# Kernel optimization log

Measured on AMD Instinct MI355X. Metric: run time of the kernel, lower is better.

Reference implementation:

```python
import jax, jax.numpy as jnp
import numpy as np

N, E, T, Q, G = 50000, 800000, 1000000, 1000000, 4096
L, H, D, HID, ED = 3, 8, 16, 128, 16
EPS = 1e-8


def setup_inputs() -> dict:
    key = jax.random.key(0)
    ks = jax.random.split(key, 20)
    inp = {
        "x": jax.random.normal(ks[0], (N, HID), jnp.float32),
        "pos": jax.random.normal(ks[1], (N, 3), jnp.float32),
        "edge_attr": jax.random.normal(ks[2], (E, ED), jnp.float32),
        "temps": jax.random.uniform(ks[3], (G, 1), jnp.float32),
        "edge_index": jax.random.randint(ks[4], (2, E), 0, N, jnp.int32),
        "triple_index": jax.random.randint(ks[5], (3, T), 0, N, jnp.int32),
        "quadra_index": jax.random.randint(ks[6], (4, Q), 0, N, jnp.int32),
        "batch": jnp.sort(jax.random.randint(ks[7], (N,), 0, G, jnp.int32)),
        "W": jax.random.normal(ks[8], (L, HID, HID), jnp.float32) * 0.08,
        "a_e": jax.random.normal(ks[9], (L, H, 2 * D + 1), jnp.float32) * 0.1,
        "a_t": jax.random.normal(ks[10], (L, H, 2 * D + 1), jnp.float32) * 0.1,
        "a_q": jax.random.normal(ks[11], (L, H, 2 * D + 1), jnp.float32) * 0.1,
        "We": jax.random.normal(ks[12], (L, ED, H), jnp.float32) * 0.1,
        "W1": jax.random.normal(ks[13], (2 * HID + 1, 256), jnp.float32) * 0.06,
        "b1": jnp.zeros((256,), jnp.float32),
        "W2": jax.random.normal(ks[14], (256, 256), jnp.float32) * 0.06,
        "b2": jnp.zeros((256,), jnp.float32),
        "W3": jax.random.normal(ks[15], (256, 1), jnp.float32) * 0.06,
        "b3": jnp.zeros((1,), jnp.float32),
    }
    return inp


def _seg_softmax(logits, seg, n):
    # numerically stable segment softmax over destination nodes
    m = jax.ops.segment_max(logits, seg, num_segments=n)
    m = jnp.where(jnp.isfinite(m), m, 0.0)
    e = jnp.exp(logits - m[seg])
    s = jax.ops.segment_sum(e, seg, num_segments=n)
    return e / (s[seg] + 1e-16)


def _hop(hh, src, dst, geom, a, bias=None):
    # hh: [N,H,D]; gather-attend-scatter for one interaction order
    q, k = hh[dst], hh[src]                      # [M,H,D]
    logits = jnp.einsum('mhd,hd->mh', q, a[:, :D]) \
           + jnp.einsum('mhd,hd->mh', k, a[:, D:2 * D]) \
           + geom[:, None] * a[:, 2 * D]
    if bias is not None:
        logits = logits + bias
    logits = jax.nn.leaky_relu(logits, 0.2)
    alpha = _seg_softmax(logits, dst, hh.shape[0])  # [M,H]
    return jax.ops.segment_sum(k * alpha[..., None], dst, num_segments=hh.shape[0])


def _geom_features(pos, edge_index, triple_index, quadra_index):
    # edge distance
    d = jnp.linalg.norm(pos[edge_index[0]] - pos[edge_index[1]] + EPS, axis=-1)
    # triple angle cos at center node j of (i,j,k)
    i, j, k = triple_index
    u, v = pos[i] - pos[j], pos[k] - pos[j]
    cos_a = (u * v).sum(-1) / (jnp.linalg.norm(u, axis=-1) * jnp.linalg.norm(v, axis=-1) + EPS)
    # quadra dihedral cos of (p0,p1,p2,p3)
    p0, p1, p2, p3 = pos[quadra_index[0]], pos[quadra_index[1]], pos[quadra_index[2]], pos[quadra_index[3]]
    b1, b2, b3 = p1 - p0, p2 - p1, p3 - p2
    n1, n2 = jnp.cross(b1, b2), jnp.cross(b2, b3)
    cos_d = (n1 * n2).sum(-1) / (jnp.linalg.norm(n1, axis=-1) * jnp.linalg.norm(n2, axis=-1) + EPS)
    return d, cos_a, cos_d


def reference(x, pos, edge_attr, temps, edge_index, triple_index, quadra_index, batch,
              W, a_e, a_t, a_q, We, W1, b1, W2, b2, W3, b3):
    d, cos_a, cos_d = _geom_features(pos, edge_index, triple_index, quadra_index)
    e_src, e_dst = edge_index[1], edge_index[0]
    t_src, t_dst = triple_index[2], triple_index[0]
    q_src, q_dst = quadra_index[3], quadra_index[0]
    h = x
    for l in range(L):
        hl = h @ W[l]                              # [N,HID]
        hh = hl.reshape(N, H, D)
        bias_e = edge_attr @ We[l]                 # [E,H]
        agg = _hop(hh, e_src, e_dst, d, a_e[l], bias_e) \
            + _hop(hh, t_src, t_dst, cos_a, a_t[l]) \
            + _hop(hh, q_src, q_dst, cos_d, a_q[l])
        h = jax.nn.elu(hl + agg.reshape(N, HID))
    # readout: sum + max pooling per graph, concat temperature scalar
    s = jax.ops.segment_sum(h, batch, num_segments=G)
    mx = jax.ops.segment_max(h, batch, num_segments=G)
    mx = jnp.where(jnp.isfinite(mx), mx, 0.0)
    mol = jnp.concatenate([s, mx, temps], axis=-1)  # [G, 2*HID+1]
    hdn = jax.nn.elu(mol @ W1 + b1)
    hdn = jax.nn.elu(hdn @ W2 + b2)
    return hdn @ W3 + b3
```

## Files before the change

### kernel.cpp

```cpp
#include <hip/hip_runtime.h>
#include <hip/hip_fp16.h>

#define NN 50000
#define EE 800000
#define TT 1000000
#define QQ 1000000
#define GG 4096
#define HID 128
#define NH 8
#define DH 16
#define CAPC 96

#define TILE 2048
#define KPT 8
#define NB 196
#define NBG 392

typedef unsigned int u32;
typedef unsigned int u32x4 __attribute__((ext_vector_type(4)));

__device__ __forceinline__ float eluf(float x){ return x > 0.f ? x : expm1f(x); }

__device__ __forceinline__ u32 pack_sg(int src, float g){
  return ((u32)src << 16) | (u32)__half_as_ushort(__float2half(g));
}

__global__ void k_count3(const int* __restrict__ ei, const int* __restrict__ ti, const int* __restrict__ qi,
                         int* __restrict__ cnt){
  int i = blockIdx.x*blockDim.x + threadIdx.x;
  if (i < EE) atomicAdd(&cnt[ei[i]], 1);
  else if (i < EE+TT) atomicAdd(&cnt[NN + ti[i-EE]], 1);
  else if (i < EE+TT+QQ) atomicAdd(&cnt[2*NN + qi[i-EE-TT]], 1);
}

__global__ __launch_bounds__(1024) void k_scan4(const int* __restrict__ cnt,
    int* __restrict__ off_e, int* __restrict__ off_t, int* __restrict__ off_q,
    int* __restrict__ cur_e, int* __restrict__ cur_t, int* __restrict__ cur_q,
    const int* __restrict__ batch, int* __restrict__ goff){
  int b = blockIdx.x, t = threadIdx.x;
  if (b == 3){
    for (int g=t; g<=GG; g+=1024){
      int lo=0, hi=NN;
      while (lo<hi){ int mid=(lo+hi)>>1; if (batch[mid]<g) lo=mid+1; else hi=mid; }
      goff[g]=lo;
    }
    return;
  }
  __shared__ int part[1024];
  const int* c = cnt + b*NN;
  int* off = (b==0)?off_e:(b==1)?off_t:off_q;
  int* cur = (b==0)?cur_e:(b==1)?cur_t:cur_q;
  int chunk = (NN + 1023) >> 10;
  int s0 = t*chunk, s1 = min(NN, s0+chunk);
  int sum = 0;
  for (int i=s0;i<s1;i++) sum += c[i];
  part[t] = sum;
  __syncthreads();
  for (int d=1; d<1024; d<<=1){
    int v = (t>=d) ? part[t-d] : 0;
    __syncthreads();
    part[t] += v;
    __syncthreads();
  }
  int run = (t==0) ? 0 : part[t-1];
  for (int i=s0;i<s1;i++){ off[i]=run; cur[i]=run; run += c[i]; }
  if (t==0) off[NN] = part[1023];
}

__global__ void k_fillE(const float* __restrict__ pos, const float* __restrict__ edge_attr,
    const int* __restrict__ ei, const float* __restrict__ We,
    int* __restrict__ cur_e, u32* __restrict__ eRec){
  int i = blockIdx.x*blockDim.x + threadIdx.x;
  if (i >= EE) return;
  int dn = ei[i], sn = ei[EE+i];
  float dx = pos[dn*3+0]-pos[sn*3+0]+1e-8f;
  float dy = pos[dn*3+1]-pos[sn*3+1]+1e-8f;
  float dz = pos[dn*3+2]-pos[sn*3+2]+1e-8f;
  float d = sqrtf(dx*dx+dy*dy+dz*dz);
  int p = atomicAdd(&cur_e[dn], 1);
  const float4* s = (const float4*)(edge_attr + (size_t)i*16);
  float4 v0=s[0], v1=s[1], v2=s[2], v3=s[3];
  float a[16] = {v0.x,v0.y,v0.z,v0.w, v1.x,v1.y,v1.z,v1.w,
                 v2.x,v2.y,v2.z,v2.w, v3.x,v3.y,v3.z,v3.w};
  u32x4 r[4];
  r[0][0] = pack_sg(sn, d); r[0][1]=0; r[0][2]=0; r[0][3]=0;
  #pragma unroll
  for (int l=0; l<3; l++){
    const float* Wel = We + l*DH*NH;
    #pragma unroll
    for (int hp=0; hp<4; hp++){
      float sa=0.f, sb=0.f;
      #pragma unroll
      for (int c=0;c<16;c++){
        sa = fmaf(a[c], Wel[c*NH + 2*hp],     sa);
        sb = fmaf(a[c], Wel[c*NH + 2*hp + 1], sb);
      }
      __half2 hh = __floats2half2_rn(sa, sb);
      r[1+l][hp] = *(u32*)&hh;
    }
  }
  u32x4* dst4 = (u32x4*)(eRec + (size_t)p*16);
  dst4[0]=r[0]; dst4[1]=r[1]; dst4[2]=r[2]; dst4[3]=r[3];
}

__global__ __launch_bounds__(256) void k_fillTQ_A(const float* __restrict__ pos,
    const int* __restrict__ ti, const int* __restrict__ qi,
    const int* __restrict__ off_t, const int* __restrict__ off_q,
    u32* __restrict__ gcur, uint2* __restrict__ stg){
  __shared__ u32 s_sg[TILE];
  __shared__ u32 s_dw[TILE];
  __shared__ u32 s_cnt[NBG];
  __shared__ u32 s_scan[512];
  __shared__ u32 s_gb[NBG];
  int t = threadIdx.x;
  size_t tile0 = (size_t)blockIdx.x * TILE;
  for (int i=t;i<NBG;i+=256) s_cnt[i]=0;
  __syncthreads();
  u32 my_sg[KPT], my_dw[KPT], my_rank[KPT]; int my_bg[KPT];
  #pragma unroll
  for (int k=0;k<KPT;k++){
    size_t idx = tile0 + (size_t)k*256 + t;
    my_bg[k] = -1;
    if (idx < (size_t)TT+QQ){
      int dst, src; float g;
      int typeq = (idx >= (size_t)TT);
      if (!typeq){
        int m = (int)idx;
        int ia=ti[m], jb=ti[TT+m], kc=ti[2*TT+m];
        float ux=pos[ia*3+0]-pos[jb*3+0], uy=pos[ia*3+1]-pos[jb*3+1], uz=pos[ia*3+2]-pos[jb*3+2];
        float vx=pos[kc*3+0]-pos[jb*3+0], vy=pos[kc*3+1]-pos[jb*3+1], vz=pos[kc*3+2]-pos[jb*3+2];
        float num = ux*vx+uy*vy+uz*vz;
        float den = sqrtf(ux*ux+uy*uy+uz*uz)*sqrtf(vx*vx+vy*vy+vz*vz) + 1e-8f;
        g = num/den; dst = ia; src = kc;
      } else {
        int m = (int)(idx - TT);
        int p0=qi[m], p1=qi[QQ+m], p2=qi[2*QQ+m], p3=qi[3*QQ+m];
        float b1x=pos[p1*3+0]-pos[p0*3+0], b1y=pos[p1*3+1]-pos[p0*3+1], b1z=pos[p1*3+2]-pos[p0*3+2];
        float b2x=pos[p2*3+0]-pos[p1*3+0], b2y=pos[p2*3+1]-pos[p1*3+1], b2z=pos[p2*3+2]-pos[p1*3+2];
        float b3x=pos[p3*3+0]-pos[p2*3+0], b3y=pos[p3*3+1]-pos[p2*3+1], b3z=pos[p3*3+2]-pos[p2*3+2];
        float n1x=b1y*b2z-b1z*b2y, n1y=b1z*b2x-b1x*b2z, n1z=b1x*b2y-b1y*b2x;
        float n2x=b2y*b3z-b2z*b3y, n2y=b2z*b3x-b2x*b3z, n2z=b2x*b3y-b2y*b3x;
        float num = n1x*n2x+n1y*n2y+n1z*n2z;
        float den = sqrtf(n1x*n1x+n1y*n1y+n1z*n1z)*sqrtf(n2x*n2x+n2y*n2y+n2z*n2z) + 1e-8f;
        g = num/den; dst = p0; src = p3;
      }
      int bg = (typeq?NB:0) + (dst>>8);
      my_sg[k] = pack_sg(src, g);
      my_dw[k] = (u32)dst | ((u32)typeq<<20);
      my_bg[k] = bg;
      my_rank[k] = atomicAdd(&s_cnt[bg], 1u);
    }
  }
  __syncthreads();
  int i0=t, i1=t+256;
  s_scan[i0] = (i0<NBG)? s_cnt[i0] : 0u;
  s_scan[i1] = (i1<NBG)? s_cnt[i1] : 0u;
  __syncthreads();
  for (int d=1; d<512; d<<=1){
    u32 a0 = (i0>=d)? s_scan[i0-d] : 0u;
    u32 a1 = (i1>=d)? s_scan[i1-d] : 0u;
    __syncthreads();
    s_scan[i0]+=a0; s_scan[i1]+=a1;
    __syncthreads();
  }
  u32 total = s_scan[NBG-1];
  #pragma unroll
  for (int k=0;k<KPT;k++){
    if (my_bg[k]>=0){
      u32 slot = s_scan[my_bg[k]] - s_cnt[my_bg[k]] + my_rank[k];
      s_sg[slot]=my_sg[k]; s_dw[slot]=my_dw[k];
    }
  }
  for (int i=t;i<NBG;i+=256)
    s_gb[i] = s_cnt[i] ? atomicAdd(&gcur[i], s_cnt[i]) : 0u;
  __syncthreads();
  for (u32 j=t; j<total; j+=256){
    u32 dw = s_dw[j];
    int typeq = (dw>>20)&1;
    int dst = dw & 0xFFFFF;
    int bg = (typeq?NB:0) + (dst>>8);
    u32 rank = j - (s_scan[bg]-s_cnt[bg]);
    int w0 = (typeq? bg-NB : bg)*256;
    size_t sbase = typeq ? (size_t)TT + (size_t)off_q[w0] : (size_t)off_t[w0];
    stg[sbase + s_gb[bg] + rank] = make_uint2(s_sg[j], dw);
  }
}

__global__ __launch_bounds__(256) void k_fillTQ_B(const uint2* __restrict__ stg,
    const int* __restrict__ off_t, const int* __restrict__ off_q,
    u32* __restrict__ csg_t, u32* __restrict__ csg_q){
  __shared__ int curL[256];
  int b = blockIdx.x, t = threadIdx.x;
  int typeq = (b>=NB);
  int bl = typeq? b-NB : b;
  const int* off = typeq? off_q : off_t;
  u32* csg = typeq? csg_q : csg_t;
  int w0 = bl*256, w1 = min(w0+256, NN);
  int s0 = off[w0], s1 = off[w1];
  for (int i=t; i<w1-w0; i+=256) curL[i] = off[w0+i];
  __syncthreads();
  size_t sb = (typeq? (size_t)TT : 0) + (size_t)s0;
  int cnt = s1 - s0;
  for (int i=t; i<cnt; i+=256){
    uint2 r = stg[sb+i];
    int dst = r.y & 0xFFFFF;
    int p = atomicAdd(&curL[dst-w0], 1);
    csg[p] = r.x;
  }
}

#define GR 16
__global__ __launch_bounds__(128) void k_gemm(const float* __restrict__ A, const float* __restrict__ W,
                                              __half* __restrict__ B16){
  int col = threadIdx.x;
  int r0 = blockIdx.x * GR;
  const float* Ab = A + (size_t)r0*HID;
  float acc[GR];
  #pragma unroll
  for (int r=0;r<GR;r++) acc[r]=0.f;
  #pragma unroll 4
  for (int k=0;k<HID;k++){
    float wv = W[k*HID+col];
    #pragma unroll
    for (int r=0;r<GR;r++) acc[r] = fmaf(Ab[r*HID+k], wv, acc[r]);
  }
  #pragma unroll
  for (int r=0;r<GR;r++) B16[(size_t)(r0+r)*HID+col] = __float2half(acc[r]);
}

__global__ void k_proj(const __half* __restrict__ hl16,
    const float* __restrict__ ae, const float* __restrict__ at, const float* __restrict__ aq,
    float* __restrict__ qa_e, float* __restrict__ ka_e,
    float* __restrict__ qa_t, float* __restrict__ ka_t,
    float* __restrict__ qa_q, float* __restrict__ ka_q){
  int i = blockIdx.x*blockDim.x + threadIdx.x;
  if (i >= NN*NH) return;
  int h = i & 7; int n = i >> 3;
  const __half2* v2 = (const __half2*)(hl16 + (size_t)n*HID + h*DH);
  float x[DH];
  #pragma unroll
  for (int d2=0; d2<8; d2++){ float2 f = __half22float2(v2[d2]); x[2*d2]=f.x; x[2*d2+1]=f.y; }
  const float* Ae = ae + h*33; const float* At_ = at + h*33; const float* Aq = aq + h*33;
  float s0=0,s1=0,s2=0,s3=0,s4=0,s5=0;
  #pragma unroll
  for (int d=0; d<DH; d++){
    s0 = fmaf(x[d], Ae[d],      s0);  s1 = fmaf(x[d], Ae[DH+d],  s1);
    s2 = fmaf(x[d], At_[d],     s2);  s3 = fmaf(x[d], At_[DH+d], s3);
    s4 = fmaf(x[d], Aq[d],      s4);  s5 = fmaf(x[d], Aq[DH+d],  s5);
  }
  qa_e[i]=s0; ka_e[i]=s1; qa_t[i]=s2; ka_t[i]=s3; qa_q[i]=s4; ka_q[i]=s5;
}

__device__ __forceinline__ void gather_acc(const __half* __restrict__ hh16,
    const int* __restrict__ srcs, const float* __restrict__ es,
    int cnt, int w, int hg, int l, float& a0, float& a1){
  int m = w;
  for (; m+8 <= cnt; m += 8){
    int s0=srcs[m], s1=srcs[m+2], s2=srcs[m+4], s3=srcs[m+6];
    float e0=es[m*NH+hg], e1=es[(m+2)*NH+hg], e2=es[(m+4)*NH+hg], e3=es[(m+6)*NH+hg];
    float2 f0 = __half22float2(*(const __half2*)&hh16[(size_t)s0*HID + 2*l]);
    float2 f1 = __half22float2(*(const __half2*)&hh16[(size_t)s1*HID + 2*l]);
    float2 f2 = __half22float2(*(const __half2*)&hh16[(size_t)s2*HID + 2*l]);
    float2 f3 = __half22float2(*(const __half2*)&hh16[(size_t)s3*HID + 2*l]);
    a0 = fmaf(f0.x, e0, a0); a1 = fmaf(f0.y, e0, a1);
    a0 = fmaf(f1.x, e1, a0); a1 = fmaf(f1.y, e1, a1);
    a0 = fmaf(f2.x, e2, a0); a1 = fmaf(f2.y, e2, a1);
    a0 = fmaf(f3.x, e3, a0); a1 = fmaf(f3.y, e3, a1);
  }
  for (; m < cnt; m += 2){
    int s0 = srcs[m];
    float e0 = es[m*NH+hg];
    float2 f0 = __half22float2(*(const __half2*)&hh16[(size_t)s0*HID + 2*l]);
    a0 = fmaf(f0.x, e0, a0); a1 = fmaf(f0.y, e0, a1);
  }
}

__global__ __launch_bounds__(128) void k_hop3(
    const int* __restrict__ off_e, const int* __restrict__ off_t, const int* __restrict__ off_q,
    const u32* __restrict__ eRec,
    const u32* __restrict__ csg_t, const u32* __restrict__ csg_q,
    const float* __restrict__ qa_e, const float* __restrict__ ka_e,
    const float* __restrict__ qa_t, const float* __restrict__ ka_t,
    const float* __restrict__ qa_q, const float* __restrict__ ka_q,
    const float* __restrict__ ae, const float* __restrict__ at, const float* __restrict__ aq,
    const __half* __restrict__ hh16, const __half* __restrict__ hlr16, float* __restrict__ hout,
    int L){
  __shared__ float sh_e[3][CAPC*NH];
  __shared__ int   sh_src[3][CAPC];
  __shared__ float sh_geom[3][CAPC];
  __shared__ float sh_s[3*NH];
  __shared__ float sh_qa[3*NH];
  __shared__ float sh_coef[3*NH];
  int n = blockIdx.x, t = threadIdx.x;
  int w = t >> 6, l = t & 63;
  if (t < 24){
    int p = t>>3, h = t&7;
    const float* a  = (p==0)?ae:(p==1)?at:aq;
    const float* qa = (p==0)?qa_e:(p==1)?qa_t:qa_q;
    sh_coef[t] = a[h*33+32];
    sh_qa[t]   = qa[n*NH+h];
    sh_s[t]    = 0.f;
  }
  int st_e = off_e[n], de = off_e[n+1]-st_e;
  int st_t = off_t[n], dt = off_t[n+1]-st_t;
  int st_q = off_q[n], dq = off_q[n+1]-st_q;
  __syncthreads();
  float aE0=0,aE1=0,aT0=0,aT1=0,aQ0=0,aQ1=0;
  int h  = t & 7;
  int hg = l >> 3;
  const __half* eRecH = (const __half*)eRec;
  int maxd = max(de, max(dt, dq));
  for (int base=0; base<maxd; base+=CAPC){
    int ce = min(CAPC, de-base); if (ce<0) ce=0;
    int ct = min(CAPC, dt-base); if (ct<0) ct=0;
    int cq = min(CAPC, dq-base); if (cq<0) cq=0;
    if (t < ce){ u32 v = eRec[(size_t)(st_e+base+t)*16]; sh_src[0][t]=(int)(v>>16); sh_geom[0][t]=__half2float(__ushort_as_half((unsigned short)(v&0xFFFFu))); }
    if (t < ct){ u32 v = csg_t[st_t+base+t]; sh_src[1][t]=(int)(v>>16); sh_geom[1][t]=__half2float(__ushort_as_half((unsigned short)(v&0xFFFFu))); }
    if (t < cq){ u32 v = csg_q[st_q+base+t]; sh_src[2][t]=(int)(v>>16); sh_geom[2][t]=__half2float(__ushort_as_half((unsigned short)(v&0xFFFFu))); }
    __syncthreads();
    float dE=0.f, dT=0.f, dQ=0.f;
    for (int i=t; i<ce*NH; i+=128){
      int m = i>>3;
      float lg = sh_qa[h] + ka_e[sh_src[0][m]*NH+h] + sh_geom[0][m]*sh_coef[h]
               + __half2float(eRecH[(size_t)(st_e+base+m)*32 + 8 + 8*L + h]);
      lg = lg>=0.f ? lg : 0.2f*lg;
      float e = __expf(lg);
      sh_e[0][i] = e; dE += e;
    }
    for (int i=t; i<ct*NH; i+=128){
      int m = i>>3;
      float lg = sh_qa[8+h] + ka_t[sh_src[1][m]*NH+h] + sh_geom[1][m]*sh_coef[8+h];
      lg = lg>=0.f ? lg : 0.2f*lg;
      float e = __expf(lg);
      sh_e[1][i] = e; dT += e;
    }
    for (int i=t; i<cq*NH; i+=128){
      int m = i>>3;
      float lg = sh_qa[16+h] + ka_q[sh_src[2][m]*NH+h] + sh_geom[2][m]*sh_coef[16+h];
      lg = lg>=0.f ? lg : 0.2f*lg;
      float e = __expf(lg);
      sh_e[2][i] = e; dQ += e;
    }
    dE += __shfl_xor(dE, 8); dE += __shfl_xor(dE, 16); dE += __shfl_xor(dE, 32);
    dT += __shfl_xor(dT, 8); dT += __shfl_xor(dT, 16); dT += __shfl_xor(dT, 32);
    dQ += __shfl_xor(dQ, 8); dQ += __shfl_xor(dQ, 16); dQ += __shfl_xor(dQ, 32);
    if (l < 8){
      atomicAdd(&sh_s[l], dE);
      atomicAdd(&sh_s[8+l], dT);
      atomicAdd(&sh_s[16+l], dQ);
    }
    __syncthreads();
    gather_acc(hh16, sh_src[0], sh_e[0], ce, w, hg, l, aE0, aE1);
    gather_acc(hh16, sh_src[1], sh_e[1], ct, w, hg, l, aT0, aT1);
    gather_acc(hh16, sh_src[2], sh_e[2], cq, w, hg, l, aQ0, aQ1);
    __syncthreads();
  }
  float* red = &sh_e[0][0];
  *(float2*)&red[(0*2+w)*128 + 2*l] = make_float2(aE0, aE1);
  *(float2*)&red[(1*2+w)*128 + 2*l] = make_float2(aT0, aT1);
  *(float2*)&red[(2*2+w)*128 + 2*l] = make_float2(aQ0, aQ1);
  __syncthreads();
  int ho = t >> 4;
  float outv = (red[t]       + red[128+t]) / (sh_s[ho]    + 1e-16f)
             + (red[256+t]   + red[384+t]) / (sh_s[8+ho]  + 1e-16f)
             + (red[512+t]   + red[640+t]) / (sh_s[16+ho] + 1e-16f);
  size_t oi = (size_t)n*HID + t;
  hout[oi] = eluf(__half2float(hlr16[oi]) + outv);
}

__global__ __launch_bounds__(128) void k_pool(const float* __restrict__ h, const int* __restrict__ goff,
                                              float* __restrict__ gs, float* __restrict__ gmx){
  int g = blockIdx.x, t = threadIdx.x;
  int s = goff[g], e = goff[g+1];
  float sum = 0.f, mx = -INFINITY;
  for (int n=s; n<e; n++){
    float v = h[(size_t)n*HID+t];
    sum += v; mx = fmaxf(mx, v);
  }
  gs[(size_t)g*HID+t] = sum;
  gmx[(size_t)g*HID+t] = (s < e) ? mx : 0.f;
}

#define GPB 8
#define MSTR 260
__global__ __launch_bounds__(256) void k_mlp(const float* __restrict__ gs, const float* __restrict__ gmx,
    const float* __restrict__ temps,
    const float* __restrict__ W1, const float* __restrict__ b1,
    const float* __restrict__ W2, const float* __restrict__ b2,
    const float* __restrict__ W3, const float* __restrict__ b3,
    float* __restrict__ out){
  __shared__ float mol[GPB][MSTR];
  __shared__ float hd[GPB][MSTR];
  int g0 = blockIdx.x*GPB, t = threadIdx.x;
  for (int i=t; i<GPB*HID; i+=256){
    int g=i>>7, d=i&127;
    mol[g][d]     = gs[(size_t)(g0+g)*HID+d];
    mol[g][128+d] = gmx[(size_t)(g0+g)*HID+d];
  }
  if (t < GPB){ mol[t][256]=temps[g0+t]; mol[t][257]=0.f; mol[t][258]=0.f; mol[t][259]=0.f; }
  __syncthreads();
  float acc[GPB];
  #pragma unroll
  for (int g=0;g<GPB;g++) acc[g]=b1[t];
  for (int k0=0;k0<256;k0+=4){
    float w0=W1[(size_t)(k0+0)*256+t], w1=W1[(size_t)(k0+1)*256+t];
    float w2=W1[(size_t)(k0+2)*256+t], w3=W1[(size_t)(k0+3)*256+t];
    #pragma unroll
    for (int g=0;g<GPB;g++){
      float4 m4 = *(const float4*)&mol[g][k0];
      acc[g] = fmaf(m4.x,w0, fmaf(m4.y,w1, fmaf(m4.z,w2, fmaf(m4.w,w3, acc[g]))));
    }
  }
  { float wl=W1[(size_t)256*256+t];
    #pragma unroll
    for (int g=0;g<GPB;g++) acc[g]=fmaf(mol[g][256],wl,acc[g]); }
  #pragma unroll
  for (int g=0;g<GPB;g++) hd[g][t]=eluf(acc[g]);
  __syncthreads();
  #pragma unroll
  for (int g=0;g<GPB;g++) acc[g]=b2[t];
  for (int k0=0;k0<256;k0+=4){
    float w0=W2[(size_t)(k0+0)*256+t], w1=W2[(size_t)(k0+1)*256+t];
    float w2=W2[(size_t)(k0+2)*256+t], w3=W2[(size_t)(k0+3)*256+t];
    #pragma unroll
    for (int g=0;g<GPB;g++){
      float4 h4 = *(const float4*)&hd[g][k0];
      acc[g] = fmaf(h4.x,w0, fmaf(h4.y,w1, fmaf(h4.z,w2, fmaf(h4.w,w3, acc[g]))));
    }
  }
  float w3v = W3[t];
  #pragma unroll
  for (int g=0;g<GPB;g++) mol[g][t] = eluf(acc[g])*w3v;
  __syncthreads();
  int g = t >> 5, j = t & 31;
  float s = 0.f;
  for (int i=j; i<256; i+=32) s += mol[g][i];
  #pragma unroll
  for (int d=16; d>0; d>>=1) s += __shfl_down(s, d, 32);
  if (j == 0) out[g0+g] = s + b3[0];
}

extern "C" void kernel_launch(void* const* d_in, const int* in_sizes, int n_in,
                              void* d_out, int out_size, void* d_ws, size_t ws_size,
                              hipStream_t stream){
  const float* x         = (const float*)d_in[0];
  const float* pos       = (const float*)d_in[1];
  const float* edge_attr = (const float*)d_in[2];
  const float* temps     = (const float*)d_in[3];
  const int*   ei        = (const int*)d_in[4];
  const int*   ti        = (const int*)d_in[5];
  const int*   qi        = (const int*)d_in[6];
  const int*   batch     = (const int*)d_in[7];
  const float* W         = (const float*)d_in[8];
  const float* a_e       = (const float*)d_in[9];
  const float* a_t       = (const float*)d_in[10];
  const float* a_q       = (const float*)d_in[11];
  const float* We        = (const float*)d_in[12];
  const float* W1        = (const float*)d_in[13];
  const float* b1        = (const float*)d_in[14];
  const float* W2        = (const float*)d_in[15];
  const float* b2        = (const float*)d_in[16];
  const float* W3        = (const float*)d_in[17];
  const float* b3        = (const float*)d_in[18];
  float* out = (float*)d_out;

  char* base = (char*)d_ws; size_t woff = 0;
  auto alloc = [&](size_t bytes)->void*{
    void* p = base + woff;
    woff = (woff + bytes + 255) & ~(size_t)255;
    return p;
  };
  float*  hbuf   = (float*)alloc((size_t)NN*HID*4);
  __half* hl16   = (__half*)alloc((size_t)NN*HID*2);
  float*  qa_e   = (float*)alloc((size_t)NN*NH*4);
  float*  ka_e   = (float*)alloc((size_t)NN*NH*4);
  float*  qa_t   = (float*)alloc((size_t)NN*NH*4);
  float*  ka_t   = (float*)alloc((size_t)NN*NH*4);
  float*  qa_q   = (float*)alloc((size_t)NN*NH*4);
  float*  ka_q   = (float*)alloc((size_t)NN*NH*4);
  u32*    eRec   = (u32*)alloc((size_t)EE*64);
  u32*    csg_t  = (u32*)alloc((size_t)TT*4);
  u32*    csg_q  = (u32*)alloc((size_t)QQ*4);
  uint2*  stg    = (uint2*)alloc((size_t)(TT+QQ)*8);
  float*  gs     = (float*)alloc((size_t)GG*HID*4);
  float*  gmx    = (float*)alloc((size_t)GG*HID*4);
  int*    cnt    = (int*)alloc((size_t)3*NN*4);
  u32*    gcur   = (u32*)alloc((size_t)NBG*4);
  int*    off_e  = (int*)alloc((size_t)(NN+1)*4);
  int*    off_t  = (int*)alloc((size_t)(NN+1)*4);
  int*    off_q  = (int*)alloc((size_t)(NN+1)*4);
  int*    cur_e  = (int*)alloc((size_t)NN*4);
  int*    cur_t  = (int*)alloc((size_t)NN*4);
  int*    cur_q  = (int*)alloc((size_t)NN*4);
  int*    goff   = (int*)alloc((size_t)(GG+1)*4);

  hipMemsetAsync(cnt, 0, (size_t)3*NN*4, stream);
  hipMemsetAsync(gcur, 0, (size_t)NBG*4, stream);
  int tot = EE+TT+QQ;
  k_count3<<<(tot+255)/256,256,0,stream>>>(ei, ti, qi, cnt);
  k_scan4<<<4,1024,0,stream>>>(cnt, off_e, off_t, off_q, cur_e, cur_t, cur_q, batch, goff);
  k_fillE<<<(EE+255)/256,256,0,stream>>>(pos, edge_attr, ei, We, cur_e, eRec);
  k_fillTQ_A<<<(TT+QQ+TILE-1)/TILE,256,0,stream>>>(pos, ti, qi, off_t, off_q, gcur, stg);
  k_fillTQ_B<<<NBG,256,0,stream>>>(stg, off_t, off_q, csg_t, csg_q);

  for (int l=0; l<3; l++){
    const float* hin = (l==0) ? x : hbuf;
    k_gemm<<<NN/GR,128,0,stream>>>(hin, W + (size_t)l*HID*HID, hl16);
    k_proj<<<(NN*NH+255)/256,256,0,stream>>>(hl16, a_e+l*264, a_t+l*264, a_q+l*264,
                                             qa_e, ka_e, qa_t, ka_t, qa_q, ka_q);
    k_hop3<<<NN,128,0,stream>>>(off_e, off_t, off_q, eRec, csg_t, csg_q,
                                qa_e, ka_e, qa_t, ka_t, qa_q, ka_q,
                                a_e+l*264, a_t+l*264, a_q+l*264,
                                hl16, hl16, hbuf, l);
  }

  k_pool<<<GG,128,0,stream>>>(hbuf, goff, gs, gmx);
  k_mlp<<<GG/GPB,256,0,stream>>>(gs, gmx, temps, W1, b1, W2, b2, W3, b3, out);
}
```

Measured before the change: 1.188 ms.

## Process each node with a single wavefront, dropping block-wide syncs in hop kernel

```diff
diff --git a/kernel.cpp b/kernel.cpp
--- a/kernel.cpp
+++ b/kernel.cpp
@@ -9,7 +9,7 @@
 #define HID 128
 #define NH 8
 #define DH 16
-#define CAPC 96
+#define CAP 64
 
 #define TILE 2048
 #define KPT 8
@@ -251,31 +251,68 @@
   qa_e[i]=s0; ka_e[i]=s1; qa_t[i]=s2; ka_t[i]=s3; qa_q[i]=s4; ka_q[i]=s5;
 }
 
-__device__ __forceinline__ void gather_acc(const __half* __restrict__ hh16,
-    const int* __restrict__ srcs, const float* __restrict__ es,
-    int cnt, int w, int hg, int l, float& a0, float& a1){
-  int m = w;
-  for (; m+8 <= cnt; m += 8){
-    int s0=srcs[m], s1=srcs[m+2], s2=srcs[m+4], s3=srcs[m+6];
-    float e0=es[m*NH+hg], e1=es[(m+2)*NH+hg], e2=es[(m+4)*NH+hg], e3=es[(m+6)*NH+hg];
-    float2 f0 = __half22float2(*(const __half2*)&hh16[(size_t)s0*HID + 2*l]);
-    float2 f1 = __half22float2(*(const __half2*)&hh16[(size_t)s1*HID + 2*l]);
-    float2 f2 = __half22float2(*(const __half2*)&hh16[(size_t)s2*HID + 2*l]);
-    float2 f3 = __half22float2(*(const __half2*)&hh16[(size_t)s3*HID + 2*l]);
-    a0 = fmaf(f0.x, e0, a0); a1 = fmaf(f0.y, e0, a1);
-    a0 = fmaf(f1.x, e1, a0); a1 = fmaf(f1.y, e1, a1);
-    a0 = fmaf(f2.x, e2, a0); a1 = fmaf(f2.y, e2, a1);
-    a0 = fmaf(f3.x, e3, a0); a1 = fmaf(f3.y, e3, a1);
-  }
-  for (; m < cnt; m += 2){
-    int s0 = srcs[m];
-    float e0 = es[m*NH+hg];
-    float2 f0 = __half22float2(*(const __half2*)&hh16[(size_t)s0*HID + 2*l]);
-    a0 = fmaf(f0.x, e0, a0); a1 = fmaf(f0.y, e0, a1);
-  }
-}
-
-__global__ __launch_bounds__(128) void k_hop3(
+template<int EB>
+__device__ __forceinline__ void hop_wave(
+    int st, int deg, const u32* __restrict__ csg, const u32* __restrict__ eRec, int L4,
+    const float* __restrict__ ka, const float* __restrict__ qa, const float* __restrict__ acoef,
+    const __half* __restrict__ hh16, float* __restrict__ sa, int n, int l, int hg,
+    float& o0, float& o1){
+  float4 qv0 = *(const float4*)(qa + (size_t)n*8);
+  float4 qv1 = *(const float4*)(qa + (size_t)n*8 + 4);
+  float qa8[8] = {qv0.x,qv0.y,qv0.z,qv0.w,qv1.x,qv1.y,qv1.z,qv1.w};
+  float cf[8];
+  #pragma unroll
+  for (int h=0;h<8;h++) cf[h] = acoef[h*33+32];
+  float acc0=0.f, acc1=0.f, dsum=0.f;
+  for (int base=0; base<deg; base+=CAP){
+    int c = min(CAP, deg-base);
+    u32 sg = 0;
+    if (l < c){
+      size_t idx = (size_t)(st+base+l);
+      float bias8[8] = {0,0,0,0,0,0,0,0};
+      if (EB){
+        sg = eRec[idx*16];
+        u32x4 br = *(const u32x4*)(eRec + idx*16 + 4 + L4);
+        #pragma unroll
+        for (int h=0;h<8;h++){
+          u32 bw = br[h>>1];
+          unsigned short us = (h&1)? (unsigned short)(bw>>16) : (unsigned short)(bw&0xFFFFu);
+          bias8[h] = __half2float(__ushort_as_half(us));
+        }
+      } else {
+        sg = csg[idx];
+      }
+      int src = (int)(sg>>16);
+      float g = __half2float(__ushort_as_half((unsigned short)(sg&0xFFFFu)));
+      float4 k0 = *(const float4*)(ka + (size_t)src*8);
+      float4 k1 = *(const float4*)(ka + (size_t)src*8 + 4);
+      float ka8[8] = {k0.x,k0.y,k0.z,k0.w,k1.x,k1.y,k1.z,k1.w};
+      #pragma unroll
+      for (int h=0;h<8;h++){
+        float lg = qa8[h] + ka8[h] + g*cf[h] + bias8[h];
+        lg = lg>=0.f ? lg : 0.2f*lg;
+        sa[l*9+h] = __expf(lg);
+      }
+    }
+    __builtin_amdgcn_wave_barrier();
+    #pragma unroll 4
+    for (int m=0; m<c; ++m){
+      float am = sa[m*9+hg];
+      u32 sv = __shfl(sg, m);
+      int src = (int)(sv>>16);
+      float2 f = __half22float2(*(const __half2*)&hh16[(size_t)src*HID + 2*l]);
+      dsum += am;
+      acc0 = fmaf(f.x, am, acc0);
+      acc1 = fmaf(f.y, am, acc1);
+    }
+    __builtin_amdgcn_wave_barrier();
+  }
+  float inv = 1.f/(dsum + 1e-16f);
+  o0 = fmaf(acc0, inv, o0);
+  o1 = fmaf(acc1, inv, o1);
+}
+
+__global__ __launch_bounds__(256) void k_hop3(
     const int* __restrict__ off_e, const int* __restrict__ off_t, const int* __restrict__ off_q,
     const u32* __restrict__ eRec,
     const u32* __restrict__ csg_t, const u32* __restrict__ csg_q,
@@ -285,87 +322,23 @@
     const float* __restrict__ ae, const float* __restrict__ at, const float* __restrict__ aq,
     const __half* __restrict__ hh16, const __half* __restrict__ hlr16, float* __restrict__ hout,
     int L){
-  __shared__ float sh_e[3][CAPC*NH];
-  __shared__ int   sh_src[3][CAPC];
-  __shared__ float sh_geom[3][CAPC];
-  __shared__ float sh_s[3*NH];
-  __shared__ float sh_qa[3*NH];
-  __shared__ float sh_coef[3*NH];
-  int n = blockIdx.x, t = threadIdx.x;
-  int w = t >> 6, l = t & 63;
-  if (t < 24){
-    int p = t>>3, h = t&7;
-    const float* a  = (p==0)?ae:(p==1)?at:aq;
-    const float* qa = (p==0)?qa_e:(p==1)?qa_t:qa_q;
-    sh_coef[t] = a[h*33+32];
-    sh_qa[t]   = qa[n*NH+h];
-    sh_s[t]    = 0.f;
-  }
-  int st_e = off_e[n], de = off_e[n+1]-st_e;
-  int st_t = off_t[n], dt = off_t[n+1]-st_t;
-  int st_q = off_q[n], dq = off_q[n+1]-st_q;
-  __syncthreads();
-  float aE0=0,aE1=0,aT0=0,aT1=0,aQ0=0,aQ1=0;
-  int h  = t & 7;
-  int hg = l >> 3;
-  const __half* eRecH = (const __half*)eRec;
-  int maxd = max(de, max(dt, dq));
-  for (int base=0; base<maxd; base+=CAPC){
-    int ce = min(CAPC, de-base); if (ce<0) ce=0;
-    int ct = min(CAPC, dt-base); if (ct<0) ct=0;
-    int cq = min(CAPC, dq-base); if (cq<0) cq=0;
-    if (t < ce){ u32 v = eRec[(size_t)(st_e+base+t)*16]; sh_src[0][t]=(int)(v>>16); sh_geom[0][t]=__half2float(__ushort_as_half((unsigned short)(v&0xFFFFu))); }
-    if (t < ct){ u32 v = csg_t[st_t+base+t]; sh_src[1][t]=(int)(v>>16); sh_geom[1][t]=__half2float(__ushort_as_half((unsigned short)(v&0xFFFFu))); }
-    if (t < cq){ u32 v = csg_q[st_q+base+t]; sh_src[2][t]=(int)(v>>16); sh_geom[2][t]=__half2float(__ushort_as_half((unsigned short)(v&0xFFFFu))); }
-    __syncthreads();
-    float dE=0.f, dT=0.f, dQ=0.f;
-    for (int i=t; i<ce*NH; i+=128){
-      int m = i>>3;
-      float lg = sh_qa[h] + ka_e[sh_src[0][m]*NH+h] + sh_geom[0][m]*sh_coef[h]
-               + __half2float(eRecH[(size_t)(st_e+base+m)*32 + 8 + 8*L + h]);
-      lg = lg>=0.f ? lg : 0.2f*lg;
-      float e = __expf(lg);
-      sh_e[0][i] = e; dE += e;
-    }
-    for (int i=t; i<ct*NH; i+=128){
-      int m = i>>3;
-      float lg = sh_qa[8+h] + ka_t[sh_src[1][m]*NH+h] + sh_geom[1][m]*sh_coef[8+h];
-      lg = lg>=0.f ? lg : 0.2f*lg;
-      float e = __expf(lg);
-      sh_e[1][i] = e; dT += e;
-    }
-    for (int i=t; i<cq*NH; i+=128){
-      int m = i>>3;
-      float lg = sh_qa[16+h] + ka_q[sh_src[2][m]*NH+h] + sh_geom[2][m]*sh_coef[16+h];
-      lg = lg>=0.f ? lg : 0.2f*lg;
-      float e = __expf(lg);
-      sh_e[2][i] = e; dQ += e;
-    }
-    dE += __shfl_xor(dE, 8); dE += __shfl_xor(dE, 16); dE += __shfl_xor(dE, 32);
-    dT += __shfl_xor(dT, 8); dT += __shfl_xor(dT, 16); dT += __shfl_xor(dT, 32);
-    dQ += __shfl_xor(dQ, 8); dQ += __shfl_xor(dQ, 16); dQ += __shfl_xor(dQ, 32);
-    if (l < 8){
-      atomicAdd(&sh_s[l], dE);
-      atomicAdd(&sh_s[8+l], dT);
-      atomicAdd(&sh_s[16+l], dQ);
-    }
-    __syncthreads();
-    gather_acc(hh16, sh_src[0], sh_e[0], ce, w, hg, l, aE0, aE1);
-    gather_acc(hh16, sh_src[1], sh_e[1], ct, w, hg, l, aT0, aT1);
-    gather_acc(hh16, sh_src[2], sh_e[2], cq, w, hg, l, aQ0, aQ1);
-    __syncthreads();
-  }
-  float* red = &sh_e[0][0];
-  *(float2*)&red[(0*2+w)*128 + 2*l] = make_float2(aE0, aE1);
-  *(float2*)&red[(1*2+w)*128 + 2*l] = make_float2(aT0, aT1);
-  *(float2*)&red[(2*2+w)*128 + 2*l] = make_float2(aQ0, aQ1);
-  __syncthreads();
-  int ho = t >> 4;
-  float outv = (red[t]       + red[128+t]) / (sh_s[ho]    + 1e-16f)
-             + (red[256+t]   + red[384+t]) / (sh_s[8+ho]  + 1e-16f)
-             + (red[512+t]   + red[640+t]) / (sh_s[16+ho] + 1e-16f);
-  size_t oi = (size_t)n*HID + t;
-  hout[oi] = eluf(__half2float(hlr16[oi]) + outv);
+  __shared__ float sh_a[4][CAP*9];
+  int t = threadIdx.x;
+  int wv = t>>6, l = t&63;
+  int n = blockIdx.x*4 + wv;
+  if (n >= NN) return;
+  float* sa = sh_a[wv];
+  int hg = l>>3;
+  float o0=0.f, o1=0.f;
+  int se = off_e[n], de = off_e[n+1]-se;
+  int st = off_t[n], dt = off_t[n+1]-st;
+  int sq = off_q[n], dq = off_q[n+1]-sq;
+  hop_wave<1>(se, de, nullptr, eRec, 4*L, ka_e, qa_e, ae, hh16, sa, n, l, hg, o0, o1);
+  hop_wave<0>(st, dt, csg_t, nullptr, 0,  ka_t, qa_t, at, hh16, sa, n, l, hg, o0, o1);
+  hop_wave<0>(sq, dq, csg_q, nullptr, 0,  ka_q, qa_q, aq, hh16, sa, n, l, hg, o0, o1);
+  size_t oi = (size_t)n*HID + 2*l;
+  float2 rf = __half22float2(*(const __half2*)&hlr16[oi]);
+  *(float2*)&hout[oi] = make_float2(eluf(rf.x + o0), eluf(rf.y + o1));
 }
 
 __global__ __launch_bounds__(128) void k_pool(const float* __restrict__ h, const int* __restrict__ goff,
@@ -508,10 +481,10 @@
     k_gemm<<<NN/GR,128,0,stream>>>(hin, W + (size_t)l*HID*HID, hl16);
     k_proj<<<(NN*NH+255)/256,256,0,stream>>>(hl16, a_e+l*264, a_t+l*264, a_q+l*264,
                                              qa_e, ka_e, qa_t, ka_t, qa_q, ka_q);
-    k_hop3<<<NN,128,0,stream>>>(off_e, off_t, off_q, eRec, csg_t, csg_q,
-                                qa_e, ka_e, qa_t, ka_t, qa_q, ka_q,
-                                a_e+l*264, a_t+l*264, a_q+l*264,
-                                hl16, hl16, hbuf, l);
+    k_hop3<<<(NN+3)/4,256,0,stream>>>(off_e, off_t, off_q, eRec, csg_t, csg_q,
+                                      qa_e, ka_e, qa_t, ka_t, qa_q, ka_q,
+                                      a_e+l*264, a_t+l*264, a_q+l*264,
+                                      hl16, hl16, hbuf, l);
   }
 
   k_pool<<<GG,128,0,stream>>>(hbuf, goff, gs, gmx);
```

Result: no change. 1.184 ms (-0.3%).
